# Kernel tuning notes

Measured on AMD Instinct MI355X. Metric: run time of the kernel, lower is better.

The kernel has to match this reference:

```python
import jax, jax.numpy as jnp
import numpy as np

OUT_H, OUT_W = 7, 7      # output_size
SCALE = 0.25             # spatial_scale
SR = 2                   # sampling_ratio


def setup_inputs() -> dict:
    key = jax.random.key(0)
    k1, k2, k3, k4 = jax.random.split(key, 4)
    B, C, T, H, W = 2, 256, 16, 64, 64
    x = jax.random.normal(k1, (B, C, T, H, W), dtype=jnp.float32)
    K = 128
    ids = jax.random.randint(k2, (K,), 0, B).astype(jnp.float32)
    xy = jax.random.uniform(k3, (K, 2), minval=0.0, maxval=200.0, dtype=jnp.float32)
    wh = jax.random.uniform(k4, (K, 2), minval=16.0, maxval=56.0, dtype=jnp.float32)
    # rois = [batch_id, x1, y1, x2, y2] as produced by convert_to_roi_format
    rois = jnp.concatenate([ids[:, None], xy, xy + wh], axis=1)
    return {"x": x, "rois": rois}


def _roi_align_3d(x, rois, out_h, out_w, scale, sr):
    """maskrcnn-benchmark style (aligned=False) RoIAlign applied to every
    temporal slice of a [B,C,T,H,W] feature map. Returns [K,C,T,out_h,out_w]."""
    B, C, T, H, W = x.shape
    Hf = jnp.float32(H)
    Wf = jnp.float32(W)

    def one_roi(roi):
        b = roi[0].astype(jnp.int32)
        feat = jnp.take(x, b, axis=0)  # [C,T,H,W]
        x1, y1, x2, y2 = roi[1] * scale, roi[2] * scale, roi[3] * scale, roi[4] * scale
        roi_w = jnp.maximum(x2 - x1, 1.0)
        roi_h = jnp.maximum(y2 - y1, 1.0)
        # sample point coordinates (sr samples per bin)
        xs = x1 + (jnp.arange(out_w * sr, dtype=jnp.float32) + 0.5) * (roi_w / (out_w * sr))
        ys = y1 + (jnp.arange(out_h * sr, dtype=jnp.float32) + 0.5) * (roi_h / (out_h * sr))
        # out-of-bounds samples contribute zero (CUDA kernel semantics)
        my = (ys >= -1.0) & (ys <= Hf)
        mx = (xs >= -1.0) & (xs <= Wf)
        yc = jnp.clip(ys, 0.0, Hf - 1.0)
        xc = jnp.clip(xs, 0.0, Wf - 1.0)
        y0 = jnp.clip(jnp.floor(yc).astype(jnp.int32), 0, H - 2)
        x0 = jnp.clip(jnp.floor(xc).astype(jnp.int32), 0, W - 2)
        ly = yc - y0.astype(jnp.float32)  # in [0,1]
        lx = xc - x0.astype(jnp.float32)
        hy, hx = 1.0 - ly, 1.0 - lx
        Y0 = y0[:, None]
        X0 = x0[None, :]
        # bilinear interpolation over all C,T at once -> [C,T,P,Q]
        v = (feat[:, :, Y0, X0] * (hy[:, None] * hx[None, :])
             + feat[:, :, Y0, X0 + 1] * (hy[:, None] * lx[None, :])
             + feat[:, :, Y0 + 1, X0] * (ly[:, None] * hx[None, :])
             + feat[:, :, Y0 + 1, X0 + 1] * (ly[:, None] * lx[None, :]))
        v = v * (my[:, None] & mx[None, :]).astype(feat.dtype)
        # average the sr x sr samples in each bin -> [C,T,out_h,out_w]
        return v.reshape(C, T, out_h, sr, out_w, sr).mean(axis=(3, 5))

    return jax.vmap(one_roi)(rois)


def reference(x, rois):
    return _roi_align_3d(x, rois, OUT_H, OUT_W, SCALE, SR)
```

## Files before the change

kernel.cpp:

```cpp
#include <hip/hip_runtime.h>


typedef float v4f __attribute__((ext_vector_type(4)));

#define PITCHB 1040

__global__ __launch_bounds__(256) void pooler_pre(const float* __restrict__ rois,
                                                  int* __restrict__ list,
                                                  int* __restrict__ jt,
                                                  uint4* __restrict__ meta) {
    __shared__ int simg[128];
    __shared__ int sorted[256];
    __shared__ int scnt[2];
    const int tid = threadIdx.x;
    if (tid < 128) simg[tid] = (int)rois[5 * tid];
    __syncthreads();
    if (tid == 0) {
        int c0 = 0, c1 = 0;
        for (int j = 0; j < 128; ++j) {
            if (simg[j] == 0) sorted[c0++] = j;
            else              sorted[128 + c1++] = j;
        }
        scnt[0] = c0; scnt[1] = c1;
        jt[0] = (c0 + 7) >> 3;
        jt[1] = (c1 + 7) >> 3;
    }
    __syncthreads();
    const int img = tid >> 7, idx = tid & 127;
    const int cnt = scnt[img];
    int k = 0;
    if (cnt > 0) k = (idx < cnt) ? sorted[(img << 7) + idx] : sorted[img << 7];
    list[tid] = k;

    float x1 = rois[5*k+1]*0.25f, y1 = rois[5*k+2]*0.25f;
    float x2 = rois[5*k+3]*0.25f, y2 = rois[5*k+4]*0.25f;
    float bw = fmaxf(x2 - x1, 1.0f) * (1.0f / 14.0f);
    float bh = fmaxf(y2 - y1, 1.0f) * (1.0f / 14.0f);
    for (int i = 0; i < 7; ++i) {
        {
            float s0 = fmaf((float)(2*i) + 0.5f, bh, y1), s1 = s0 + bh;
            float m0 = (s0 >= -1.f && s0 <= 64.f) ? 1.f : 0.f;
            float m1 = (s1 >= -1.f && s1 <= 64.f) ? 1.f : 0.f;
            float c0 = fminf(fmaxf(s0, 0.f), 63.f), c1 = fminf(fmaxf(s1, 0.f), 63.f);
            int i0 = min((int)c0, 62), i1 = min((int)c1, 62);
            float l0 = c0 - (float)i0, l1 = c1 - (float)i1;
            float h0 = (1.f - l0) * m0, L0 = l0 * m0;
            float h1 = (1.f - l1) * m1, L1 = l1 * m1;
            bool d = (i1 != i0);
            float w0 = h0 + (d ? 0.f : h1);
            float w1 = L0 + (d ? h1 : L1);
            float w2 = d ? L1 : 0.f;
            int b = i0;
            if (i0 > 61) { b = 61; w2 = w1; w1 = w0; w0 = 0.f; }
            uint4 e;
            e.x = __float_as_uint(w0); e.y = __float_as_uint(w1);
            e.z = __float_as_uint(w2); e.w = (unsigned)b;
            meta[tid * 14 + i] = e;
        }
        {
            float s0 = fmaf((float)(2*i) + 0.5f, bw, x1), s1 = s0 + bw;
            float m0 = (s0 >= -1.f && s0 <= 64.f) ? 0.25f : 0.f;
            float m1 = (s1 >= -1.f && s1 <= 64.f) ? 0.25f : 0.f;
            float c0 = fminf(fmaxf(s0, 0.f), 63.f), c1 = fminf(fmaxf(s1, 0.f), 63.f);
            int i0 = min((int)c0, 62), i1 = min((int)c1, 62);
            float l0 = c0 - (float)i0, l1 = c1 - (float)i1;
            float h0 = (1.f - l0) * m0, L0 = l0 * m0;
            float h1 = (1.f - l1) * m1, L1 = l1 * m1;
            bool d = (i1 != i0);
            float w0 = h0 + (d ? 0.f : h1);
            float w1 = L0 + (d ? h1 : L1);
            float w2 = d ? L1 : 0.f;
            int b = i0;
            if (i0 > 61) { b = 61; w2 = w1; w1 = w0; w0 = 0.f; }
            uint4 e;
            e.x = __float_as_uint(w0); e.y = __float_as_uint(w1);
            e.z = __float_as_uint(w2); e.w = (unsigned)b;
            meta[tid * 14 + 7 + i] = e;
        }
    }
}

__global__ __launch_bounds__(512, 4) void pooler_main(const float* __restrict__ x,
                                                      const int* __restrict__ list,
                                                      const int* __restrict__ jt,
                                                      const uint4* __restrict__ meta,
                                                      float* __restrict__ out) {
    __shared__ __align__(16) char lds[64 * PITCHB];

    const int tid = threadIdx.x;
    const int bid = blockIdx.x;
    const int th  = bid & 1;
    const int c   = (bid >> 1) & 255;
    const int img = bid >> 9;
    const int sbase = img << 7;
    const int jtn = jt[img];

    const int lane = tid & 63, wave = tid >> 6;
    const int o  = lane;
    const int oc = o < 49 ? o : 48;
    const int ph = oc / 7, pw = oc - ph * 7;

    const float* gbase = x + (((size_t)((img << 8) + c)) << 16) + ((size_t)th << 15);

    float buf[32];
    #pragma unroll
    for (int m = 0; m < 8; ++m) {
        int n = tid + (m << 9);
        #pragma unroll
        for (int t = 0; t < 4; ++t) buf[m * 4 + t] = gbase[t * 4096 + n];
    }

    for (int i = 0; i < 2; ++i) {
        __syncthreads();
        #pragma unroll
        for (int m = 0; m < 8; ++m) {
            int n = tid + (m << 9);
            int y = n >> 6, xx = n & 63;
            *(v4f*)(lds + y * PITCHB + ((xx + ((y >> 1) & 1)) << 4)) =
                v4f{buf[m*4], buf[m*4+1], buf[m*4+2], buf[m*4+3]};
        }
        __syncthreads();
        if (i == 0) {
            #pragma unroll
            for (int m = 0; m < 8; ++m) {
                int n = tid + (m << 9);
                #pragma unroll
                for (int t = 0; t < 4; ++t) buf[m*4+t] = gbase[16384 + t * 4096 + n];
            }
        }
        if (jtn > 0) {
            const int tb = (th << 3) + (i << 2);
            int s0 = sbase + wave;
            int k0 = list[s0];
            uint4 ye0 = meta[s0 * 14 + ph];
            uint4 xe0 = meta[s0 * 14 + 7 + pw];
            for (int j = 0; j < jtn; ++j) {
                int sn = sbase + wave + (min(j + 1, jtn - 1) << 3);
                int k1 = list[sn];
                uint4 ye1 = meta[sn * 14 + ph];
                uint4 xe1 = meta[sn * 14 + 7 + pw];

                float yw0 = __uint_as_float(ye0.x);
                float yw1 = __uint_as_float(ye0.y);
                float yw2 = __uint_as_float(ye0.z);
                float xw0 = __uint_as_float(xe0.x);
                float xw1 = __uint_as_float(xe0.y);
                float xw2 = __uint_as_float(xe0.z);
                int yb = (int)ye0.w, xb = (int)xe0.w;

                int r0 = yb, r1 = yb + 1, r2 = yb + 2;
                const char* p0 = lds + r0 * PITCHB + ((xb + ((r0 >> 1) & 1)) << 4);
                const char* p1 = lds + r1 * PITCHB + ((xb + ((r1 >> 1) & 1)) << 4);
                const char* p2 = lds + r2 * PITCHB + ((xb + ((r2 >> 1) & 1)) << 4);
                v4f a0 = *(const v4f*)p0, a1 = *(const v4f*)(p0+16), a2 = *(const v4f*)(p0+32);
                v4f b0 = *(const v4f*)p1, b1 = *(const v4f*)(p1+16), b2 = *(const v4f*)(p1+32);
                v4f c0 = *(const v4f*)p2, c1 = *(const v4f*)(p2+16), c2 = *(const v4f*)(p2+32);
                v4f t0 = a0 * xw0 + a1 * xw1 + a2 * xw2;
                v4f t1 = b0 * xw0 + b1 * xw1 + b2 * xw2;
                v4f t2 = c0 * xw0 + c1 * xw1 + c2 * xw2;
                v4f acc = t0 * yw0 + t1 * yw1 + t2 * yw2;

                if (o < 49) {
                    float* po = out + (size_t)k0 * 200704 + (size_t)((c << 4) + tb) * 49 + o;
                    po[0]   = acc.x;
                    po[49]  = acc.y;
                    po[98]  = acc.z;
                    po[147] = acc.w;
                }
                k0 = k1; ye0 = ye1; xe0 = xe1;
            }
        }
    }
}

extern "C" void kernel_launch(void* const* d_in, const int* in_sizes, int n_in,
                              void* d_out, int out_size, void* d_ws, size_t ws_size,
                              hipStream_t stream) {
    const float* x    = (const float*)d_in[0];
    const float* rois = (const float*)d_in[1];
    float* out = (float*)d_out;
    int*   list = (int*)d_ws;
    int*   jtp  = (int*)((char*)d_ws + 1024);
    uint4* meta = (uint4*)((char*)d_ws + 2048);
    pooler_pre<<<1, 256, 0, stream>>>(rois, list, jtp, meta);
    pooler_main<<<1024, 512, 0, stream>>>(x, list, jtp, meta, out);
}
```

Baseline: 63.21 us.

## Store feature tiles in LDS as bf16 to halve shared memory and raise occupancy

Feature values are packed to bf16 (round-to-nearest-even) before being written to LDS. This halves the LDS tile size (pitch 1040 to 520 bytes) and lets launch bounds request 8 blocks per SM instead of 4. The register double-buffered prefetch of the next time chunk is dropped in favour of loading directly per iteration. The bilinear combine now uses nine precomputed 2D weights on unpacked bf16 values. This trades accuracy, since inputs are rounded to bf16, for higher occupancy and less LDS traffic.

Result: slower. 89.48 us (+41.6%).

```diff
diff --git a/kernel.cpp b/kernel.cpp
--- a/kernel.cpp
+++ b/kernel.cpp
@@ -1,9 +1,7 @@
 #include <hip/hip_runtime.h>
 
 
-typedef float v4f __attribute__((ext_vector_type(4)));
-
-#define PITCHB 1040
+#define PITCHB 520
 
 __global__ __launch_bounds__(256) void pooler_pre(const float* __restrict__ rois,
                                                   int* __restrict__ list,
@@ -80,7 +78,17 @@
     }
 }
 
-__global__ __launch_bounds__(512, 4) void pooler_main(const float* __restrict__ x,
+__device__ __forceinline__ unsigned bfrne(float f) {
+    unsigned u = __float_as_uint(f);
+    return (u + 0x7FFFu + ((u >> 16) & 1u)) >> 16;
+}
+__device__ __forceinline__ unsigned pack2(float lo, float hi) {
+    return bfrne(lo) | (bfrne(hi) << 16);
+}
+__device__ __forceinline__ float bflo(unsigned w) { return __uint_as_float(w << 16); }
+__device__ __forceinline__ float bfhi(unsigned w) { return __uint_as_float(w & 0xFFFF0000u); }
+
+__global__ __launch_bounds__(512, 8) void pooler_main(const float* __restrict__ x,
                                                       const int* __restrict__ list,
                                                       const int* __restrict__ jt,
                                                       const uint4* __restrict__ meta,
@@ -102,32 +110,21 @@
 
     const float* gbase = x + (((size_t)((img << 8) + c)) << 16) + ((size_t)th << 15);
 
-    float buf[32];
-    #pragma unroll
-    for (int m = 0; m < 8; ++m) {
-        int n = tid + (m << 9);
-        #pragma unroll
-        for (int t = 0; t < 4; ++t) buf[m * 4 + t] = gbase[t * 4096 + n];
-    }
-
     for (int i = 0; i < 2; ++i) {
         __syncthreads();
-        #pragma unroll
-        for (int m = 0; m < 8; ++m) {
-            int n = tid + (m << 9);
-            int y = n >> 6, xx = n & 63;
-            *(v4f*)(lds + y * PITCHB + ((xx + ((y >> 1) & 1)) << 4)) =
-                v4f{buf[m*4], buf[m*4+1], buf[m*4+2], buf[m*4+3]};
-        }
-        __syncthreads();
-        if (i == 0) {
+        {
+            const float* pb = gbase + (i << 14);
             #pragma unroll
             for (int m = 0; m < 8; ++m) {
                 int n = tid + (m << 9);
-                #pragma unroll
-                for (int t = 0; t < 4; ++t) buf[m*4+t] = gbase[16384 + t * 4096 + n];
+                float v0 = pb[n], v1 = pb[4096 + n], v2 = pb[8192 + n], v3 = pb[12288 + n];
+                uint2 ch;
+                ch.x = pack2(v0, v1);
+                ch.y = pack2(v2, v3);
+                *(uint2*)(lds + (n >> 6) * PITCHB + ((n & 63) << 3)) = ch;
             }
         }
+        __syncthreads();
         if (jtn > 0) {
             const int tb = (th << 3) + (i << 2);
             int s0 = sbase + wave;
@@ -148,24 +145,47 @@
                 float xw2 = __uint_as_float(xe0.z);
                 int yb = (int)ye0.w, xb = (int)xe0.w;
 
-                int r0 = yb, r1 = yb + 1, r2 = yb + 2;
-                const char* p0 = lds + r0 * PITCHB + ((xb + ((r0 >> 1) & 1)) << 4);
-                const char* p1 = lds + r1 * PITCHB + ((xb + ((r1 >> 1) & 1)) << 4);
-                const char* p2 = lds + r2 * PITCHB + ((xb + ((r2 >> 1) & 1)) << 4);
-                v4f a0 = *(const v4f*)p0, a1 = *(const v4f*)(p0+16), a2 = *(const v4f*)(p0+32);
-                v4f b0 = *(const v4f*)p1, b1 = *(const v4f*)(p1+16), b2 = *(const v4f*)(p1+32);
-                v4f c0 = *(const v4f*)p2, c1 = *(const v4f*)(p2+16), c2 = *(const v4f*)(p2+32);
-                v4f t0 = a0 * xw0 + a1 * xw1 + a2 * xw2;
-                v4f t1 = b0 * xw0 + b1 * xw1 + b2 * xw2;
-                v4f t2 = c0 * xw0 + c1 * xw1 + c2 * xw2;
-                v4f acc = t0 * yw0 + t1 * yw1 + t2 * yw2;
+                const char* p0 = lds + yb * PITCHB + (xb << 3);
+                float w00 = yw0*xw0, w01 = yw0*xw1, w02 = yw0*xw2;
+                float w10 = yw1*xw0, w11 = yw1*xw1, w12 = yw1*xw2;
+                float w20 = yw2*xw0, w21 = yw2*xw1, w22 = yw2*xw2;
+
+                uint2 q00 = *(const uint2*)(p0);
+                uint2 q01 = *(const uint2*)(p0 + 8);
+                uint2 q02 = *(const uint2*)(p0 + 16);
+                uint2 q10 = *(const uint2*)(p0 + PITCHB);
+                uint2 q11 = *(const uint2*)(p0 + PITCHB + 8);
+                uint2 q12 = *(const uint2*)(p0 + PITCHB + 16);
+                uint2 q20 = *(const uint2*)(p0 + 2 * PITCHB);
+                uint2 q21 = *(const uint2*)(p0 + 2 * PITCHB + 8);
+                uint2 q22 = *(const uint2*)(p0 + 2 * PITCHB + 16);
+
+                float a0, a1, a2, a3;
+                a0  = bflo(q00.x) * w00; a1  = bfhi(q00.x) * w00;
+                a2  = bflo(q00.y) * w00; a3  = bfhi(q00.y) * w00;
+                a0 += bflo(q01.x) * w01; a1 += bfhi(q01.x) * w01;
+                a2 += bflo(q01.y) * w01; a3 += bfhi(q01.y) * w01;
+                a0 += bflo(q02.x) * w02; a1 += bfhi(q02.x) * w02;
+                a2 += bflo(q02.y) * w02; a3 += bfhi(q02.y) * w02;
+                a0 += bflo(q10.x) * w10; a1 += bfhi(q10.x) * w10;
+                a2 += bflo(q10.y) * w10; a3 += bfhi(q10.y) * w10;
+                a0 += bflo(q11.x) * w11; a1 += bfhi(q11.x) * w11;
+                a2 += bflo(q11.y) * w11; a3 += bfhi(q11.y) * w11;
+                a0 += bflo(q12.x) * w12; a1 += bfhi(q12.x) * w12;
+                a2 += bflo(q12.y) * w12; a3 += bfhi(q12.y) * w12;
+                a0 += bflo(q20.x) * w20; a1 += bfhi(q20.x) * w20;
+                a2 += bflo(q20.y) * w20; a3 += bfhi(q20.y) * w20;
+                a0 += bflo(q21.x) * w21; a1 += bfhi(q21.x) * w21;
+                a2 += bflo(q21.y) * w21; a3 += bfhi(q21.y) * w21;
+                a0 += bflo(q22.x) * w22; a1 += bfhi(q22.x) * w22;
+                a2 += bflo(q22.y) * w22; a3 += bfhi(q22.y) * w22;
 
                 if (o < 49) {
                     float* po = out + (size_t)k0 * 200704 + (size_t)((c << 4) + tb) * 49 + o;
-                    po[0]   = acc.x;
-                    po[49]  = acc.y;
-                    po[98]  = acc.z;
-                    po[147] = acc.w;
+                    po[0]   = a0;
+                    po[49]  = a1;
+                    po[98]  = a2;
+                    po[147] = a3;
                 }
                 k0 = k1; ye0 = ye1; xe0 = xe1;
             }
```

## Stage all 16 time slices as bf16 in LDS and stage output stores

Applied to the files above, without the earlier changes.

Each block now handles one (image, channel) pair with all 16 temporal slices. The feature map is packed to bf16 pairs in dynamic LDS, about 130KB plus a per-wave output staging area, and the grid is halved. Results are staged in LDS so each wave writes the 784 contiguous floats per ROI/channel as float4 stores instead of scattered scalar stores. This trades fp32 accuracy for bf16 rounding of the inputs, and the larger LDS footprint reduces occupancy.

New measurement: 64.82 us. +2.5%, slower.

```diff
diff --git a/kernel.cpp b/kernel.cpp
--- a/kernel.cpp
+++ b/kernel.cpp
@@ -1,9 +1,8 @@
 #include <hip/hip_runtime.h>
 
 
-typedef float v4f __attribute__((ext_vector_type(4)));
-
-#define PITCHB 1040
+#define LDS_B  66560
+#define LDS_OB 133120
 
 __global__ __launch_bounds__(256) void pooler_pre(const float* __restrict__ rois,
                                                   int* __restrict__ list,
@@ -80,18 +79,27 @@
     }
 }
 
-__global__ __launch_bounds__(512, 4) void pooler_main(const float* __restrict__ x,
+__device__ __forceinline__ unsigned bfrne(float f) {
+    unsigned u = __float_as_uint(f);
+    return (u + 0x7FFFu + ((u >> 16) & 1u)) >> 16;
+}
+__device__ __forceinline__ unsigned pack2(float lo, float hi) {
+    return bfrne(lo) | (bfrne(hi) << 16);
+}
+__device__ __forceinline__ float bflo(unsigned w) { return __uint_as_float(w << 16); }
+__device__ __forceinline__ float bfhi(unsigned w) { return __uint_as_float(w & 0xFFFF0000u); }
+
+__global__ __launch_bounds__(512, 2) void pooler_main(const float* __restrict__ x,
                                                       const int* __restrict__ list,
                                                       const int* __restrict__ jt,
                                                       const uint4* __restrict__ meta,
                                                       float* __restrict__ out) {
-    __shared__ __align__(16) char lds[64 * PITCHB];
+    extern __shared__ __align__(16) char smem[];
 
     const int tid = threadIdx.x;
     const int bid = blockIdx.x;
-    const int th  = bid & 1;
-    const int c   = (bid >> 1) & 255;
-    const int img = bid >> 9;
+    const int c   = bid & 255;
+    const int img = bid >> 8;
     const int sbase = img << 7;
     const int jtn = jt[img];
 
@@ -100,75 +108,102 @@
     const int oc = o < 49 ? o : 48;
     const int ph = oc / 7, pw = oc - ph * 7;
 
-    const float* gbase = x + (((size_t)((img << 8) + c)) << 16) + ((size_t)th << 15);
-
-    float buf[32];
-    #pragma unroll
+    const float* gb = x + ((size_t)((img << 8) + c) << 16);
+    #pragma unroll 2
     for (int m = 0; m < 8; ++m) {
         int n = tid + (m << 9);
-        #pragma unroll
-        for (int t = 0; t < 4; ++t) buf[m * 4 + t] = gbase[t * 4096 + n];
-    }
-
-    for (int i = 0; i < 2; ++i) {
-        __syncthreads();
-        #pragma unroll
-        for (int m = 0; m < 8; ++m) {
-            int n = tid + (m << 9);
-            int y = n >> 6, xx = n & 63;
-            *(v4f*)(lds + y * PITCHB + ((xx + ((y >> 1) & 1)) << 4)) =
-                v4f{buf[m*4], buf[m*4+1], buf[m*4+2], buf[m*4+3]};
-        }
-        __syncthreads();
-        if (i == 0) {
+        float v0  = gb[n];
+        float v1  = gb[(1  << 12) + n];
+        float v2  = gb[(2  << 12) + n];
+        float v3  = gb[(3  << 12) + n];
+        float v4  = gb[(4  << 12) + n];
+        float v5  = gb[(5  << 12) + n];
+        float v6  = gb[(6  << 12) + n];
+        float v7  = gb[(7  << 12) + n];
+        float v8  = gb[(8  << 12) + n];
+        float v9  = gb[(9  << 12) + n];
+        float v10 = gb[(10 << 12) + n];
+        float v11 = gb[(11 << 12) + n];
+        float v12 = gb[(12 << 12) + n];
+        float v13 = gb[(13 << 12) + n];
+        float v14 = gb[(14 << 12) + n];
+        float v15 = gb[(15 << 12) + n];
+        uint4 qa, qb;
+        qa.x = pack2(v0,  v1);  qa.y = pack2(v2,  v3);
+        qa.z = pack2(v4,  v5);  qa.w = pack2(v6,  v7);
+        qb.x = pack2(v8,  v9);  qb.y = pack2(v10, v11);
+        qb.z = pack2(v12, v13); qb.w = pack2(v14, v15);
+        int y = n >> 6, xx = n & 63;
+        int off = ((y * 65 + xx) << 4);
+        *(uint4*)(smem + off)         = qa;
+        *(uint4*)(smem + LDS_B + off) = qb;
+    }
+    __syncthreads();
+
+    if (jtn > 0) {
+        float* ob = (float*)(smem + LDS_OB + wave * 3136);
+        int s0 = sbase + wave;
+        int k0 = list[s0];
+        uint4 ye0 = meta[s0 * 14 + ph];
+        uint4 xe0 = meta[s0 * 14 + 7 + pw];
+        for (int j = 0; j < jtn; ++j) {
+            int sn = sbase + wave + (min(j + 1, jtn - 1) << 3);
+            int k1 = list[sn];
+            uint4 ye1 = meta[sn * 14 + ph];
+            uint4 xe1 = meta[sn * 14 + 7 + pw];
+
+            float yw0 = __uint_as_float(ye0.x);
+            float yw1 = __uint_as_float(ye0.y);
+            float yw2 = __uint_as_float(ye0.z);
+            float xw0 = __uint_as_float(xe0.x);
+            float xw1 = __uint_as_float(xe0.y);
+            float xw2 = __uint_as_float(xe0.z);
+            int yb = (int)ye0.w, xb = (int)xe0.w;
+
+            float a0=0.f,a1=0.f,a2=0.f,a3=0.f,a4=0.f,a5=0.f,a6=0.f,a7=0.f;
+            float a8=0.f,a9=0.f,a10=0.f,a11=0.f,a12=0.f,a13=0.f,a14=0.f,a15=0.f;
+            const char* pA = smem + ((yb * 65 + xb) << 4);
             #pragma unroll
-            for (int m = 0; m < 8; ++m) {
-                int n = tid + (m << 9);
+            for (int r = 0; r < 3; ++r) {
+                float wr = (r == 0) ? yw0 : ((r == 1) ? yw1 : yw2);
+                const char* rowA = pA + r * (65 * 16);
                 #pragma unroll
-                for (int t = 0; t < 4; ++t) buf[m*4+t] = gbase[16384 + t * 4096 + n];
+                for (int cc = 0; cc < 3; ++cc) {
+                    float w = wr * ((cc == 0) ? xw0 : ((cc == 1) ? xw1 : xw2));
+                    uint4 qa = *(const uint4*)(rowA + (cc << 4));
+                    uint4 qb = *(const uint4*)(rowA + LDS_B + (cc << 4));
+                    a0  += bflo(qa.x) * w;  a1  += bfhi(qa.x) * w;
+                    a2  += bflo(qa.y) * w;  a3  += bfhi(qa.y) * w;
+                    a4  += bflo(qa.z) * w;  a5  += bfhi(qa.z) * w;
+                    a6  += bflo(qa.w) * w;  a7  += bfhi(qa.w) * w;
+                    a8  += bflo(qb.x) * w;  a9  += bfhi(qb.x) * w;
+                    a10 += bflo(qb.y) * w;  a11 += bfhi(qb.y) * w;
+                    a12 += bflo(qb.z) * w;  a13 += bfhi(qb.z) * w;
+                    a14 += bflo(qb.w) * w;  a15 += bfhi(qb.w) * w;
+                }
             }
-        }
-        if (jtn > 0) {
-            const int tb = (th << 3) + (i << 2);
-            int s0 = sbase + wave;
-            int k0 = list[s0];
-            uint4 ye0 = meta[s0 * 14 + ph];
-            uint4 xe0 = meta[s0 * 14 + 7 + pw];
-            for (int j = 0; j < jtn; ++j) {
-                int sn = sbase + wave + (min(j + 1, jtn - 1) << 3);
-                int k1 = list[sn];
-                uint4 ye1 = meta[sn * 14 + ph];
-                uint4 xe1 = meta[sn * 14 + 7 + pw];
-
-                float yw0 = __uint_as_float(ye0.x);
-                float yw1 = __uint_as_float(ye0.y);
-                float yw2 = __uint_as_float(ye0.z);
-                float xw0 = __uint_as_float(xe0.x);
-                float xw1 = __uint_as_float(xe0.y);
-                float xw2 = __uint_as_float(xe0.z);
-                int yb = (int)ye0.w, xb = (int)xe0.w;
-
-                int r0 = yb, r1 = yb + 1, r2 = yb + 2;
-                const char* p0 = lds + r0 * PITCHB + ((xb + ((r0 >> 1) & 1)) << 4);
-                const char* p1 = lds + r1 * PITCHB + ((xb + ((r1 >> 1) & 1)) << 4);
-                const char* p2 = lds + r2 * PITCHB + ((xb + ((r2 >> 1) & 1)) << 4);
-                v4f a0 = *(const v4f*)p0, a1 = *(const v4f*)(p0+16), a2 = *(const v4f*)(p0+32);
-                v4f b0 = *(const v4f*)p1, b1 = *(const v4f*)(p1+16), b2 = *(const v4f*)(p1+32);
-                v4f c0 = *(const v4f*)p2, c1 = *(const v4f*)(p2+16), c2 = *(const v4f*)(p2+32);
-                v4f t0 = a0 * xw0 + a1 * xw1 + a2 * xw2;
-                v4f t1 = b0 * xw0 + b1 * xw1 + b2 * xw2;
-                v4f t2 = c0 * xw0 + c1 * xw1 + c2 * xw2;
-                v4f acc = t0 * yw0 + t1 * yw1 + t2 * yw2;
-
-                if (o < 49) {
-                    float* po = out + (size_t)k0 * 200704 + (size_t)((c << 4) + tb) * 49 + o;
-                    po[0]   = acc.x;
-                    po[49]  = acc.y;
-                    po[98]  = acc.z;
-                    po[147] = acc.w;
+            if (o < 49) {
+                ob[ 0*49 + o] = a0;   ob[ 1*49 + o] = a1;
+                ob[ 2*49 + o] = a2;   ob[ 3*49 + o] = a3;
+                ob[ 4*49 + o] = a4;   ob[ 5*49 + o] = a5;
+                ob[ 6*49 + o] = a6;   ob[ 7*49 + o] = a7;
+                ob[ 8*49 + o] = a8;   ob[ 9*49 + o] = a9;
+                ob[10*49 + o] = a10;  ob[11*49 + o] = a11;
+                ob[12*49 + o] = a12;  ob[13*49 + o] = a13;
+                ob[14*49 + o] = a14;  ob[15*49 + o] = a15;
+            }
+            asm volatile("s_waitcnt lgkmcnt(0)" ::: "memory");
+            __builtin_amdgcn_sched_barrier(0);
+            float* gdst = out + (size_t)k0 * 200704 + (size_t)c * 784;
+            #pragma unroll
+            for (int rr = 0; rr < 4; ++rr) {
+                int i4 = lane + (rr << 6);
+                if (i4 < 196) {
+                    float4 v = *(const float4*)(ob + (i4 << 2));
+                    *(float4*)(gdst + (i4 << 2)) = v;
                 }
-                k0 = k1; ye0 = ye1; xe0 = xe1;
             }
+            k0 = k1; ye0 = ye1; xe0 = xe1;
         }
     }
 }
@@ -182,6 +217,9 @@
     int*   list = (int*)d_ws;
     int*   jtp  = (int*)((char*)d_ws + 1024);
     uint4* meta = (uint4*)((char*)d_ws + 2048);
+    static const int LDS_BYTES = 133120 + 8 * 3136;
+    hipFuncSetAttribute((const void*)pooler_main,
+                        hipFuncAttributeMaxDynamicSharedMemorySize, LDS_BYTES);
     pooler_pre<<<1, 256, 0, stream>>>(rois, list, jtp, meta);
-    pooler_main<<<1024, 512, 0, stream>>>(x, list, jtp, meta, out);
-}
+    pooler_main<<<512, 512, LDS_BYTES, stream>>>(x, list, jtp, meta, out);
+}
```
